# Kernel tuning notes

Measured on AMD Instinct MI355X. Metric: run time of the kernel, lower is better.

Reference implementation:

```python
import jax, jax.numpy as jnp
import numpy as np


def setup_inputs() -> dict:
    key = jax.random.key(0)
    ks = jax.random.split(key, 14)
    B, Ld, Lq, D = 64, 512, 128, 512
    d_node = jax.random.normal(ks[0], (B, Ld, D), jnp.float32)
    q_node = jax.random.normal(ks[1], (B, Lq, D), jnp.float32)
    qq_graph = jax.random.randint(ks[2], (B, Lq, Lq), 0, 2, jnp.int32)
    dq_graph = jax.random.randint(ks[3], (B, Ld, Lq), 0, 2, jnp.int32)
    dd_graph = jax.random.randint(ks[4], (B, Ld, Ld), 0, 2, jnp.int32)
    qd_graph = jax.random.randint(ks[5], (B, Lq, Ld), 0, 2, jnp.int32)
    s = 0.02
    W_nw = jax.random.normal(ks[6], (1, D), jnp.float32) * s
    b_nw = jnp.zeros((1,), jnp.float32)
    W_self = jax.random.normal(ks[7], (D, D), jnp.float32) * s
    b_self = jnp.zeros((D,), jnp.float32)
    W_dd = jax.random.normal(ks[8], (D, D), jnp.float32) * s
    W_qq = jax.random.normal(ks[9], (D, D), jnp.float32) * s
    W_dq = jax.random.normal(ks[10], (D, D), jnp.float32) * s
    W_qd = jax.random.normal(ks[11], (D, D), jnp.float32) * s
    return {"d_node": d_node, "q_node": q_node, "qq_graph": qq_graph,
            "dq_graph": dq_graph, "dd_graph": dd_graph, "qd_graph": qd_graph,
            "W_nw": W_nw, "b_nw": b_nw, "W_self": W_self, "b_self": b_self,
            "W_dd": W_dd, "W_qq": W_qq, "W_dq": W_dq, "W_qd": W_qd,
            "iteration_steps": 2}


def reference(d_node, q_node, qq_graph, dq_graph, dd_graph, qd_graph,
              W_nw, b_nw, W_self, b_self, W_dd, W_qq, W_dq, W_qd,
              iteration_steps):
    dd = dd_graph.astype(jnp.float32)
    dq = dq_graph.astype(jnp.float32)
    qq = qq_graph.astype(jnp.float32)
    qd = qd_graph.astype(jnp.float32)

    # neighbor counts, clamped to 1 where a node has no neighbors
    d_nb = dd.sum(-1) + dq.sum(-1)              # [B, Ld]
    d_nb = jnp.where(d_nb >= 1.0, d_nb, 1.0)
    q_nb = qq.sum(-1) + qd.sum(-1)              # [B, Lq]
    q_nb = jnp.where(q_nb >= 1.0, q_nb, 1.0)

    all_d_w, all_q_w = [], []
    for _ in range(iteration_steps):
        d_w = jax.nn.sigmoid(jnp.einsum('bld,od->blo', d_node, W_nw) + b_nw)[..., 0]  # [B, Ld]
        q_w = jax.nn.sigmoid(jnp.einsum('bld,od->blo', q_node, W_nw) + b_nw)[..., 0]  # [B, Lq]
        all_d_w.append(d_w)
        all_q_w.append(q_w)

        self_d = jnp.einsum('bld,od->blo', d_node, W_self) + b_self
        self_q = jnp.einsum('bld,od->blo', q_node, W_self) + b_self
        dd_info = jnp.einsum('bld,od->blo', d_node, W_dd)
        qd_info = jnp.einsum('bld,od->blo', d_node, W_qd)
        qq_info = jnp.einsum('bld,od->blo', q_node, W_qq)
        dq_info = jnp.einsum('bld,od->blo', q_node, W_dq)

        # masked weights: graph is 0/1, so replace_masked_values(., graph, 0) == graph * weight
        dd_msg = jnp.einsum('bij,bjd->bid', dd * d_w[:, None, :], dd_info)  # [B,Ld,D]
        qd_msg = jnp.einsum('bij,bjd->bid', qd * d_w[:, None, :], qd_info)  # [B,Lq,D]
        qq_msg = jnp.einsum('bij,bjd->bid', qq * q_w[:, None, :], qq_info)  # [B,Lq,D]
        dq_msg = jnp.einsum('bij,bjd->bid', dq * q_w[:, None, :], dq_info)  # [B,Ld,D]

        agg_q = (qq_msg + qd_msg) / q_nb[..., None]
        agg_d = (dd_msg + dq_msg) / d_nb[..., None]
        d_node = jax.nn.relu(self_d + agg_d)
        q_node = jax.nn.relu(self_q + agg_q)

    all_d_w = jnp.stack(all_d_w, axis=1)  # [B, steps, Ld]
    all_q_w = jnp.stack(all_q_w, axis=1)  # [B, steps, Lq]
    return (d_node, q_node, all_d_w, all_q_w)
```

## Files before the change

### kernel.cpp

```cpp
#include <hip/hip_runtime.h>
#include <cstdint>
#include <cstddef>

typedef _Float16 h16;
typedef __attribute__((ext_vector_type(8))) _Float16 h16x8;
typedef __attribute__((ext_vector_type(4))) _Float16 h16x4;
typedef __attribute__((ext_vector_type(4))) float f32x4;

constexpr int B_ = 64, LD = 512, LQ = 128, DIM = 512, STEPS = 2;
constexpr int MD = B_ * LD;
constexpr int MQ = B_ * LQ;
constexpr int KST = LD + LQ;
constexpr int KAGG = KST + DIM;

#define ASYNC16(gp, lp)                                                          \
  __builtin_amdgcn_global_load_lds(                                              \
      (const __attribute__((address_space(1))) unsigned int*)(gp),               \
      (__attribute__((address_space(3))) unsigned int*)(lp), 16, 0, 0)

struct Src {
  const h16* p0; int s0; long bstr0;
  const h16* p1; int s1; long bstr1;
  int ksplit;
};

template <int WM, int WN, class Epi>
__device__ __forceinline__ void gemm_body(int b, long tileM, long tileN,
                                          Src sa, Src sb, int K,
                                          const Epi& epi, h16* lds) {
  constexpr int BM = WM * 32;
  constexpr int BN = WN * 64;
  constexpr int AE = BM * 32;
  constexpr int BUFE = (BM + BN) * 32;
  constexpr int NA = BM / 128;
  constexpr int NB = BN / 128;
  constexpr int LT = NA + NB;
  constexpr int HM = WM / 2;

  const int tid = threadIdx.x;
  const int lane = tid & 63;
  const int wv = tid >> 6;
  const int wr = wv >> 2, wc = wv & 3;
  const int quad = lane >> 4, l16 = lane & 15;

  const int u = tid & 255;
  const int sb2 = tid >> 8;
  const int r = u >> 2;
  const int es = (r ^ (r >> 2)) & 3;
  const int kq = (u & 3) ^ es;

  const h16* pa[2][NA];
  const h16* pb[2][NB];
#pragma unroll
  for (int s = 0; s < NA; s++) {
    const long row = tileM + sb2 * 64 + r + 128 * s;
    pa[0][s] = sa.p0 + (size_t)b * sa.bstr0 + row * (long)sa.s0 + kq * 8;
    pa[1][s] = sa.p1 + (size_t)b * sa.bstr1 + row * (long)sa.s1 + kq * 8 - sa.ksplit;
  }
#pragma unroll
  for (int s = 0; s < NB; s++) {
    const long row = tileN + sb2 * 64 + r + 128 * s;
    pb[0][s] = sb.p0 + (size_t)b * sb.bstr0 + row * (long)sb.s0 + kq * 8;
    pb[1][s] = sb.p1 + (size_t)b * sb.bstr1 + row * (long)sb.s1 + kq * 8 - sb.ksplit;
  }

  const int ef = (l16 ^ (l16 >> 2)) & 3;
  int offA[WM], offB[WN];
#pragma unroll
  for (int i = 0; i < WM; i++) {
    const int row = wr * (WM * 16) + i * 16 + l16;
    offA[i] = (row * 4 + (quad ^ ef)) * 8;
  }
#pragma unroll
  for (int j = 0; j < WN; j++) {
    const int row = wc * (WN * 16) + j * 16 + l16;
    offB[j] = AE + (row * 4 + (quad ^ ef)) * 8;
  }

  f32x4 acc[WM][WN] = {};
  const int T = K >> 5;

  auto dmaA = [&](int t, int off) {
    const int k0 = t * 32;
    h16* base = lds + off + tid * 8;
    const int sel = (k0 >= sa.ksplit);
#pragma unroll
    for (int s = 0; s < NA; s++) ASYNC16(pa[sel][s] + k0, base + 4096 * s);
  };
  auto dmaB = [&](int t, int off) {
    const int k0 = t * 32;
    h16* base = lds + off + AE + tid * 8;
    const int sel = (k0 >= sb.ksplit);
#pragma unroll
    for (int s = 0; s < NB; s++) ASYNC16(pb[sel][s] + k0, base + 4096 * s);
  };

  h16x8 bf[WN];
  auto phase0 = [&](int off) {
    h16x8 af[HM];
#pragma unroll
    for (int j = 0; j < WN; j++) bf[j] = *(const h16x8*)(lds + off + offB[j]);
#pragma unroll
    for (int i = 0; i < HM; i++) af[i] = *(const h16x8*)(lds + off + offA[i]);
    __builtin_amdgcn_s_setprio(1);
#pragma unroll
    for (int i = 0; i < HM; i++)
#pragma unroll
      for (int j = 0; j < WN; j++)
        acc[i][j] = __builtin_amdgcn_mfma_f32_16x16x32_f16(af[i], bf[j], acc[i][j], 0, 0, 0);
    __builtin_amdgcn_s_setprio(0);
  };
  auto phase1 = [&](int off) {
    h16x8 af[WM - HM];
#pragma unroll
    for (int i = 0; i < WM - HM; i++) af[i] = *(const h16x8*)(lds + off + offA[HM + i]);
    __builtin_amdgcn_s_setprio(1);
#pragma unroll
    for (int i = 0; i < WM - HM; i++)
#pragma unroll
      for (int j = 0; j < WN; j++)
        acc[HM + i][j] = __builtin_amdgcn_mfma_f32_16x16x32_f16(af[i], bf[j], acc[HM + i][j], 0, 0, 0);
    __builtin_amdgcn_s_setprio(0);
  };

  dmaA(0, 0); dmaB(0, 0);
  dmaA(1, BUFE); dmaB(1, BUFE);

  int co = 0;
  int no = 2 * BUFE;
  for (int t = 0; t < T - 1; ++t) {
    if constexpr (LT == 4) asm volatile("s_waitcnt vmcnt(4)" ::: "memory");
    else                   asm volatile("s_waitcnt vmcnt(2)" ::: "memory");
    __builtin_amdgcn_s_barrier();
    asm volatile("" ::: "memory");
    __builtin_amdgcn_sched_barrier(0);
    if (t + 2 < T) dmaA(t + 2, no);
    phase0(co);
    __builtin_amdgcn_s_barrier();
    asm volatile("" ::: "memory");
    __builtin_amdgcn_sched_barrier(0);
    if (t + 2 < T) dmaB(t + 2, no);
    phase1(co);
    co = (co == 2 * BUFE) ? 0 : co + BUFE;
    no = (no == 2 * BUFE) ? 0 : no + BUFE;
  }
  asm volatile("s_waitcnt vmcnt(0)" ::: "memory");
  __builtin_amdgcn_s_barrier();
  asm volatile("" ::: "memory");
  __builtin_amdgcn_sched_barrier(0);
  phase0(co);
  __builtin_amdgcn_s_barrier();
  asm volatile("" ::: "memory");
  __builtin_amdgcn_sched_barrier(0);
  phase1(co);

#pragma unroll
  for (int i = 0; i < WM; i++) {
#pragma unroll
    for (int j = 0; j < WN; j++) {
      const int gm0 = (int)tileM + wr * (WM * 16) + i * 16 + quad * 4;
      const int gn  = (int)tileN + wc * (WN * 16) + j * 16 + l16;
#pragma unroll
      for (int rr = 0; rr < 4; rr++) epi(b, gm0 + rr, gn, acc[i][j][rr]);
    }
  }
}

struct EpiDense {
  const float* w;
  h16* stackA;
  h16* stackB;
  int lnShift;
  int offA, offB;
  __device__ void operator()(int, int gm, int gn, float v) const {
    const int b = gn >> lnShift, l = gn & ((1 << lnShift) - 1);
    const h16 sv = (h16)(w[gn] * v);
    if (gm < 512)
      stackA[((size_t)b * 512 + gm) * 640 + offA + l] = sv;
    else
      stackB[((size_t)b * 512 + (gm - 512)) * 640 + offB + l] = sv;
  }
};
struct EpiAgg {
  const float* bias;
  float* out;
  h16* nodeNext;
  int rowsPerB;
  __device__ void operator()(int b, int gm, int gn, float v) const {
    const size_t row = (size_t)b * rowsPerB + gm;
    const float val = fmaxf(v + bias[gn], 0.f);
    if (out) out[row * 512 + gn] = val;
    if (nodeNext) nodeNext[row * 512 + gn] = (h16)val;
  }
};

__global__ __launch_bounds__(512, 2) void k_dense(Src saD, Src sbD, EpiDense epiD,
                                                  Src saQ, Src sbQ, EpiDense epiQ) {
  __shared__ __align__(16) h16 lds[3 * (256 * 32 + 256 * 32)];
  const int g = blockIdx.x;
  const int x = g / 160;
  const int yy = g % 160;
  if (yy < 128)
    gemm_body<8, 4>(0, (long)x * 256, (long)yy * 256, saD, sbD, 512, epiD, lds);
  else
    gemm_body<8, 4>(0, (long)x * 256, (long)(yy - 128) * 256, saQ, sbQ, 512, epiQ, lds);
}

__global__ __launch_bounds__(512, 2) void k_agg(Src saD, Src sbD, EpiAgg epiD,
                                                Src saQ, Src sbQ, EpiAgg epiQ) {
  __shared__ __align__(16) h16 lds[3 * (256 * 32 + 256 * 32)];
  const int g = blockIdx.x;
  const int b = g & 63;
  const int unit = g >> 6;
  if (unit < 4)
    gemm_body<8, 4>(b, (long)(unit >> 1) * 256, (long)(unit & 1) * 256, saD, sbD, KAGG, epiD, lds);
  else
    gemm_body<4, 2>(b, 0L, (long)(unit - 4) * 128, saQ, sbQ, KAGG, epiQ, lds);
}

__global__ __launch_bounds__(256) void k_convert(const float* __restrict__ dn,
                                                 const float* __restrict__ qn,
                                                 h16* __restrict__ dnb,
                                                 h16* __restrict__ qnb) {
  const size_t i4 = ((size_t)blockIdx.x * 256 + threadIdx.x) * 4;
  constexpr size_t TD = (size_t)MD * DIM;
  const float* src; h16* dst; size_t idx;
  if (i4 < TD) { src = dn; dst = dnb; idx = i4; }
  else         { src = qn; dst = qnb; idx = i4 - TD; }
  const float4 v = *(const float4*)&src[idx];
  h16x4 o; o.x = (h16)v.x; o.y = (h16)v.y; o.z = (h16)v.z; o.w = (h16)v.w;
  *(h16x4*)&dst[idx] = o;
}

__global__ __launch_bounds__(256) void k_wcat(const float* __restrict__ Wself,
                                              const float* __restrict__ Wdd,
                                              const float* __restrict__ Wqd,
                                              const float* __restrict__ Wqq,
                                              const float* __restrict__ Wdq,
                                              h16* __restrict__ catD,
                                              h16* __restrict__ catQ) {
  const int i = blockIdx.x * 256 + threadIdx.x;
  float vD, vQ;
  if (i < 512 * 512)       { vD = Wself[i];            vQ = vD; }
  else if (i < 1024 * 512) { vD = Wdd[i - 512 * 512];  vQ = Wqq[i - 512 * 512]; }
  else                     { vD = Wqd[i - 1024 * 512]; vQ = Wdq[i - 1024 * 512]; }
  catD[i] = (h16)vD; catQ[i] = (h16)vQ;
}

__global__ __launch_bounds__(256) void k_maskD(const int* __restrict__ dd,
                                               const int* __restrict__ dq,
                                               h16* __restrict__ maskD) {
  const int row = blockIdx.x * 4 + (threadIdx.x >> 6);
  const int lane = threadIdx.x & 63;
  const int* pdd = dd + (size_t)row * 512;
  const int* pdq = dq + (size_t)row * 128;
  h16* pm = maskD + (size_t)row * 640;
  float vals[10];
  float s = 0.f;
#pragma unroll
  for (int t = 0; t < 10; t++) {
    const int j = lane + t * 64;
    const float v = (float)((j < 512) ? pdd[j] : pdq[j - 512]);
    vals[t] = v; s += v;
  }
  for (int m = 32; m; m >>= 1) s += __shfl_xor(s, m);
  const float inv = 1.f / fmaxf(s, 1.f);
#pragma unroll
  for (int t = 0; t < 10; t++) pm[lane + t * 64] = (h16)(vals[t] * inv);
}

__global__ __launch_bounds__(256) void k_maskQ(const int* __restrict__ qq,
                                               const int* __restrict__ qd,
                                               h16* __restrict__ maskQ) {
  const int row = blockIdx.x * 4 + (threadIdx.x >> 6);
  const int lane = threadIdx.x & 63;
  const int* pqq = qq + (size_t)row * 128;
  const int* pqd = qd + (size_t)row * 512;
  h16* pm = maskQ + (size_t)row * 640;
  float vals[10];
  float s = 0.f;
#pragma unroll
  for (int t = 0; t < 10; t++) {
    const int j = lane + t * 64;
    const float v = (float)((j < 128) ? pqq[j] : pqd[j - 128]);
    vals[t] = v; s += v;
  }
  for (int m = 32; m; m >>= 1) s += __shfl_xor(s, m);
  const float inv = 1.f / fmaxf(s, 1.f);
#pragma unroll
  for (int t = 0; t < 10; t++) pm[lane + t * 64] = (h16)(vals[t] * inv);
}

__global__ __launch_bounds__(256) void k_w(const h16* __restrict__ dnb,
                                           const h16* __restrict__ qnb,
                                           const float* __restrict__ Wnw,
                                           const float* __restrict__ bnw,
                                           float* __restrict__ d_w,
                                           float* __restrict__ q_w,
                                           float* __restrict__ adw,
                                           float* __restrict__ aqw, int it) {
  const int row = blockIdx.x * 4 + (threadIdx.x >> 6);
  const int lane = threadIdx.x & 63;
  const bool isD = row < MD;
  const h16* node = isD ? dnb + (size_t)row * 512 : qnb + (size_t)(row - MD) * 512;
  const h16x8 v = *(const h16x8*)&node[lane * 8];
  const float4 w0 = *(const float4*)&Wnw[lane * 8];
  const float4 w1 = *(const float4*)&Wnw[lane * 8 + 4];
  float s = (float)v[0] * w0.x + (float)v[1] * w0.y + (float)v[2] * w0.z +
            (float)v[3] * w0.w + (float)v[4] * w1.x + (float)v[5] * w1.y +
            (float)v[6] * w1.z + (float)v[7] * w1.w;
  for (int m = 32; m; m >>= 1) s += __shfl_xor(s, m);
  if (lane == 0) {
    const float w = 1.f / (1.f + expf(-(s + bnw[0])));
    if (isD) {
      d_w[row] = w;
      adw[((size_t)(row >> 9) * STEPS + it) * 512 + (row & 511)] = w;
    } else {
      const int rq = row - MD;
      q_w[rq] = w;
      aqw[((size_t)(rq >> 7) * STEPS + it) * 128 + (rq & 127)] = w;
    }
  }
}

extern "C" void kernel_launch(void* const* d_in, const int* in_sizes, int n_in,
                              void* d_out, int out_size, void* d_ws, size_t ws_size,
                              hipStream_t stream) {
  (void)in_sizes; (void)n_in; (void)out_size; (void)ws_size;

  const float* d_node = (const float*)d_in[0];
  const float* q_node = (const float*)d_in[1];
  const int*   qq     = (const int*)d_in[2];
  const int*   dq     = (const int*)d_in[3];
  const int*   dd     = (const int*)d_in[4];
  const int*   qd     = (const int*)d_in[5];
  const float* W_nw   = (const float*)d_in[6];
  const float* b_nw   = (const float*)d_in[7];
  const float* W_self = (const float*)d_in[8];
  const float* b_self = (const float*)d_in[9];
  const float* W_dd   = (const float*)d_in[10];
  const float* W_qq   = (const float*)d_in[11];
  const float* W_dq   = (const float*)d_in[12];
  const float* W_qd   = (const float*)d_in[13];

  float* outd = (float*)d_out;
  float* outq = outd + (size_t)MD * DIM;
  float* adw  = outq + (size_t)MQ * DIM;
  float* aqw  = adw + (size_t)B_ * STEPS * LD;

  char* p = (char*)d_ws;
  auto alloc = [&](size_t bytes) { char* r = p; p += (bytes + 255) & ~(size_t)255; return r; };
  h16* dnode[2], *qnode[2];
  dnode[0] = (h16*)alloc((size_t)MD * DIM * 2);
  dnode[1] = (h16*)alloc((size_t)MD * DIM * 2);
  qnode[0] = (h16*)alloc((size_t)MQ * DIM * 2);
  qnode[1] = (h16*)alloc((size_t)MQ * DIM * 2);
  h16* catD    = (h16*)alloc((size_t)1536 * 512 * 2);
  h16* catQ    = (h16*)alloc((size_t)1536 * 512 * 2);
  h16* maskD   = (h16*)alloc((size_t)B_ * LD * KST * 2);
  h16* maskQ   = (h16*)alloc((size_t)B_ * LQ * KST * 2);
  h16* stackDT = (h16*)alloc((size_t)B_ * 512 * KST * 2);
  h16* stackQT = (h16*)alloc((size_t)B_ * 512 * KST * 2);
  float* d_wb  = (float*)alloc((size_t)MD * 4);
  float* q_wb  = (float*)alloc((size_t)MQ * 4);

  k_convert<<<dim3((MD * DIM + MQ * DIM) / 4 / 256), 256, 0, stream>>>(d_node, q_node, dnode[0], qnode[0]);
  k_wcat<<<dim3(1536 * 512 / 256), 256, 0, stream>>>(W_self, W_dd, W_qd, W_qq, W_dq, catD, catQ);
  k_maskD<<<dim3(MD / 4), 256, 0, stream>>>(dd, dq, maskD);
  k_maskQ<<<dim3(MQ / 4), 256, 0, stream>>>(qq, qd, maskQ);

  for (int it = 0; it < STEPS; it++) {
    const bool last = (it == STEPS - 1);
    h16* ncur_d = dnode[it & 1];
    h16* nnext_d = dnode[(it & 1) ^ 1];
    h16* ncur_q = qnode[it & 1];
    h16* nnext_q = qnode[(it & 1) ^ 1];

    k_w<<<dim3((MD + MQ) / 4), 256, 0, stream>>>(ncur_d, ncur_q, W_nw, b_nw, d_wb, q_wb, adw, aqw, it);

    {
      Src saD{catD + 512 * 512, 512, 0, catD + 512 * 512, 512, 0, 512};
      Src sbD{ncur_d, 512, 0, ncur_d, 512, 0, 512};
      Src saQ{catQ + 512 * 512, 512, 0, catQ + 512 * 512, 512, 0, 512};
      Src sbQ{ncur_q, 512, 0, ncur_q, 512, 0, 512};
      k_dense<<<dim3(640), 512, 0, stream>>>(
          saD, sbD, EpiDense{d_wb, stackDT, stackQT, 9, 0, 128},
          saQ, sbQ, EpiDense{q_wb, stackQT, stackDT, 7, 0, 512});
    }
    {
      Src saD{maskD, 640, (long)LD * KST, ncur_d, 512, (long)LD * DIM, KST};
      Src sbD{stackDT, 640, (long)512 * KST, catD, 512, 0, KST};
      Src saQ{maskQ, 640, (long)LQ * KST, ncur_q, 512, (long)LQ * DIM, KST};
      Src sbQ{stackQT, 640, (long)512 * KST, catQ, 512, 0, KST};
      k_agg<<<dim3(512), 512, 0, stream>>>(
          saD, sbD, EpiAgg{b_self, last ? outd : nullptr, last ? nullptr : nnext_d, 512},
          saQ, sbQ, EpiAgg{b_self, last ? outq : nullptr, last ? nullptr : nnext_q, 128});
    }
  }
}
```

Baseline: 569.0 us.

## Restructure GEMM main loop into ping-pong schedule with split LDS reads and MFMA phases

```diff
diff --git a/kernel.cpp b/kernel.cpp
--- a/kernel.cpp
+++ b/kernel.cpp
@@ -34,7 +34,6 @@
   constexpr int BUFE = (BM + BN) * 32;
   constexpr int NA = BM / 128;
   constexpr int NB = BN / 128;
-  constexpr int LT = NA + NB;
   constexpr int HM = WM / 2;
 
   const int tid = threadIdx.x;
@@ -95,64 +94,62 @@
     for (int s = 0; s < NB; s++) ASYNC16(pb[sel][s] + k0, base + 4096 * s);
   };
 
-  h16x8 bf[WN];
-  auto phase0 = [&](int off) {
-    h16x8 af[HM];
-#pragma unroll
-    for (int j = 0; j < WN; j++) bf[j] = *(const h16x8*)(lds + off + offB[j]);
-#pragma unroll
-    for (int i = 0; i < HM; i++) af[i] = *(const h16x8*)(lds + off + offA[i]);
-    __builtin_amdgcn_s_setprio(1);
-#pragma unroll
-    for (int i = 0; i < HM; i++)
-#pragma unroll
-      for (int j = 0; j < WN; j++)
-        acc[i][j] = __builtin_amdgcn_mfma_f32_16x16x32_f16(af[i], bf[j], acc[i][j], 0, 0, 0);
-    __builtin_amdgcn_s_setprio(0);
-  };
-  auto phase1 = [&](int off) {
-    h16x8 af[WM - HM];
-#pragma unroll
-    for (int i = 0; i < WM - HM; i++) af[i] = *(const h16x8*)(lds + off + offA[HM + i]);
-    __builtin_amdgcn_s_setprio(1);
-#pragma unroll
-    for (int i = 0; i < WM - HM; i++)
-#pragma unroll
-      for (int j = 0; j < WN; j++)
-        acc[HM + i][j] = __builtin_amdgcn_mfma_f32_16x16x32_f16(af[i], bf[j], acc[HM + i][j], 0, 0, 0);
-    __builtin_amdgcn_s_setprio(0);
-  };
+  h16x8 af0[HM], af1[WM - HM], bf[WN];
 
   dmaA(0, 0); dmaB(0, 0);
   dmaA(1, BUFE); dmaB(1, BUFE);
+  if constexpr (NA == 2) asm volatile("s_waitcnt vmcnt(4)" ::: "memory");
+  else                   asm volatile("s_waitcnt vmcnt(2)" ::: "memory");
+  __builtin_amdgcn_s_barrier();
 
   int co = 0;
   int no = 2 * BUFE;
-  for (int t = 0; t < T - 1; ++t) {
-    if constexpr (LT == 4) asm volatile("s_waitcnt vmcnt(4)" ::: "memory");
-    else                   asm volatile("s_waitcnt vmcnt(2)" ::: "memory");
+  for (int t = 0; t < T; ++t) {
+    const bool pf = (t + 2 < T);
+#pragma unroll
+    for (int j = 0; j < WN; j++) bf[j] = *(const h16x8*)(lds + co + offB[j]);
+#pragma unroll
+    for (int i = 0; i < HM; i++) af0[i] = *(const h16x8*)(lds + co + offA[i]);
+    if (pf) dmaA(t + 2, no);
+    __builtin_amdgcn_sched_barrier(0);
     __builtin_amdgcn_s_barrier();
-    asm volatile("" ::: "memory");
-    __builtin_amdgcn_sched_barrier(0);
-    if (t + 2 < T) dmaA(t + 2, no);
-    phase0(co);
+    asm volatile("s_waitcnt lgkmcnt(0)" ::: "memory");
+    __builtin_amdgcn_sched_barrier(0);
+    __builtin_amdgcn_s_setprio(1);
+#pragma unroll
+    for (int i = 0; i < HM; i++)
+#pragma unroll
+      for (int j = 0; j < WN; j++)
+        acc[i][j] = __builtin_amdgcn_mfma_f32_16x16x32_f16(af0[i], bf[j], acc[i][j], 0, 0, 0);
+    __builtin_amdgcn_s_setprio(0);
+    __builtin_amdgcn_sched_barrier(0);
     __builtin_amdgcn_s_barrier();
-    asm volatile("" ::: "memory");
-    __builtin_amdgcn_sched_barrier(0);
-    if (t + 2 < T) dmaB(t + 2, no);
-    phase1(co);
+    if (pf) {
+      if constexpr (NA == 2) asm volatile("s_waitcnt vmcnt(2)" ::: "memory");
+      else                   asm volatile("s_waitcnt vmcnt(1)" ::: "memory");
+    } else {
+      asm volatile("s_waitcnt vmcnt(0)" ::: "memory");
+    }
+#pragma unroll
+    for (int i = 0; i < WM - HM; i++) af1[i] = *(const h16x8*)(lds + co + offA[HM + i]);
+    if (pf) dmaB(t + 2, no);
+    __builtin_amdgcn_sched_barrier(0);
+    __builtin_amdgcn_s_barrier();
+    asm volatile("s_waitcnt lgkmcnt(0)" ::: "memory");
+    __builtin_amdgcn_sched_barrier(0);
+    __builtin_amdgcn_s_setprio(1);
+#pragma unroll
+    for (int i = 0; i < WM - HM; i++)
+#pragma unroll
+      for (int j = 0; j < WN; j++)
+        acc[HM + i][j] = __builtin_amdgcn_mfma_f32_16x16x32_f16(af1[i], bf[j], acc[HM + i][j], 0, 0, 0);
+    __builtin_amdgcn_s_setprio(0);
+    __builtin_amdgcn_sched_barrier(0);
+    __builtin_amdgcn_s_barrier();
+
     co = (co == 2 * BUFE) ? 0 : co + BUFE;
     no = (no == 2 * BUFE) ? 0 : no + BUFE;
   }
-  asm volatile("s_waitcnt vmcnt(0)" ::: "memory");
-  __builtin_amdgcn_s_barrier();
-  asm volatile("" ::: "memory");
-  __builtin_amdgcn_sched_barrier(0);
-  phase0(co);
-  __builtin_amdgcn_s_barrier();
-  asm volatile("" ::: "memory");
-  __builtin_amdgcn_sched_barrier(0);
-  phase1(co);
 
 #pragma unroll
   for (int i = 0; i < WM; i++) {
```

Measured after the change: 576.4 us. No clear change (+1.3%).
